# Kernel optimization log

Hardware: AMD Instinct MI355X
Metric: run time of the kernel (lower is better)

Reference implementation:

```python
import jax, jax.numpy as jnp
import numpy as np

B, D, T = 16384, 1024, 128  # batch, embed_dim, num_degradation_types
V, L = 4, 3                 # variants per sample, degradations per variant


def setup_inputs() -> dict:
    key = jax.random.key(0)
    k1, k2, k3, k4 = jax.random.split(key, 4)
    clean_embeddings = jax.random.normal(k1, (B, D), dtype=jnp.float32)
    W = jax.random.normal(k2, (T, D), dtype=jnp.float32) * (1.0 / np.sqrt(D))
    b = jnp.zeros((T,), dtype=jnp.float32)
    deg_indices = jax.random.randint(k3, (B, V, L), 0, T, dtype=jnp.int32)
    deg_mask = jax.random.randint(k4, (B, V, L), 0, 2, dtype=jnp.int32)
    return {"clean_embeddings": clean_embeddings, "W": W, "b": b,
            "deg_indices": deg_indices, "deg_mask": deg_mask}


def reference(clean_embeddings, W, b, deg_indices, deg_mask):
    # Linear + softmax: [B, T]
    logits = jnp.einsum("bd,td->bt", clean_embeddings, W) + b
    probs = jax.nn.softmax(logits, axis=-1)
    # Gather probs at each (batch, label) pair: [B, V*L] -> [B, V, L]
    flat_idx = deg_indices.reshape(B, V * L)
    gathered = jnp.take_along_axis(probs, flat_idx, axis=1).reshape(B, V, L)
    # Masked sum over all labels of a sample, divided by max(num_variants, 1)=V
    per_sample = (gathered * deg_mask.astype(probs.dtype)).sum(axis=(1, 2)) / V
    return per_sample.sum() / B
```

## Files before the change

kernel.cpp:

```cpp
#include <hip/hip_runtime.h>

#define B_SIZE 16384
#define D_DIM  1024
#define T_DIM  128
#define VLn    12
#define ROWS   16
#define KPW    256
#define NCHUNK 8

typedef __attribute__((ext_vector_type(8))) short  short8;
typedef __attribute__((ext_vector_type(4))) float  f32x4;

__device__ __forceinline__ unsigned short f2bf(float f) {
    union { float f; unsigned int u; } c; c.f = f;
    unsigned int u = c.u;
    return (unsigned short)((u + 0x7FFFu + ((u >> 16) & 1u)) >> 16);
}

__global__ __launch_bounds__(256)
void conv_w_kernel(const float* __restrict__ W, unsigned short* __restrict__ Wb) {
    const int i = (blockIdx.x * 256 + threadIdx.x) * 4;
    const float4 v = *(const float4*)(W + i);
    ushort4 h; h.x = f2bf(v.x); h.y = f2bf(v.y); h.z = f2bf(v.z); h.w = f2bf(v.w);
    *(ushort4*)(Wb + i) = h;
}

__global__ __launch_bounds__(256, 4)
void qloss_kernel(const float* __restrict__ emb,
                  const unsigned short* __restrict__ Wb,
                  const float* __restrict__ bias,
                  const int*   __restrict__ didx,
                  const int*   __restrict__ dmsk,
                  float*       __restrict__ out)
{
    __shared__ float sP[4 * 16 * 132 + 4];
    const int t    = threadIdx.x;
    const int w    = t >> 6;
    const int lane = t & 63;
    const int m15  = lane & 15;
    const int quad = lane >> 4;
    const int r0   = blockIdx.x * ROWS;

    f32x4 acc[8];
#pragma unroll
    for (int ct = 0; ct < 8; ++ct) acc[ct] = (f32x4){0.f, 0.f, 0.f, 0.f};

    const float*          aptr = emb + (size_t)(r0 + m15) * D_DIM + w * KPW + quad * 8;
    const unsigned short* bptr = Wb  + (size_t)m15 * D_DIM        + w * KPW + quad * 8;

#pragma unroll 2
    for (int kc = 0; kc < NCHUNK; ++kc) {
        const int ko = kc * 32;
        const float4 a0 = *(const float4*)(aptr + ko);
        const float4 a1 = *(const float4*)(aptr + ko + 4);
        short8 bf[8];
#pragma unroll
        for (int ct = 0; ct < 8; ++ct)
            bf[ct] = *(const short8*)(bptr + (size_t)ct * 16 * D_DIM + ko);
        short8 a;
        a[0] = (short)f2bf(a0.x); a[1] = (short)f2bf(a0.y);
        a[2] = (short)f2bf(a0.z); a[3] = (short)f2bf(a0.w);
        a[4] = (short)f2bf(a1.x); a[5] = (short)f2bf(a1.y);
        a[6] = (short)f2bf(a1.z); a[7] = (short)f2bf(a1.w);
#pragma unroll
        for (int ct = 0; ct < 8; ++ct)
            acc[ct] = __builtin_amdgcn_mfma_f32_16x16x32_bf16(a, bf[ct], acc[ct], 0, 0, 0);
    }

#pragma unroll
    for (int ct = 0; ct < 8; ++ct)
#pragma unroll
        for (int i = 0; i < 4; ++i)
            sP[w * 2112 + (quad * 4 + i) * 132 + ct * 16 + m15] = acc[ct][i];
    __syncthreads();

    const int row = t >> 4;
    const int s   = t & 15;
    {
        float v[8];
#pragma unroll
        for (int j = 0; j < 8; ++j) v[j] = bias[s * 8 + j];
#pragma unroll
        for (int w2 = 0; w2 < 4; ++w2) {
            const float4 p0 = *(const float4*)&sP[w2 * 2112 + row * 132 + s * 8];
            const float4 p1 = *(const float4*)&sP[w2 * 2112 + row * 132 + s * 8 + 4];
            v[0] += p0.x; v[1] += p0.y; v[2] += p0.z; v[3] += p0.w;
            v[4] += p1.x; v[5] += p1.y; v[6] += p1.z; v[7] += p1.w;
        }
        float m = -1e30f;
#pragma unroll
        for (int j = 0; j < 8; ++j) m = fmaxf(m, v[j]);
#pragma unroll
        for (int off = 1; off < 16; off <<= 1) m = fmaxf(m, __shfl_xor(m, off));
        float ssum = 0.f;
#pragma unroll
        for (int j = 0; j < 8; ++j) { v[j] = __expf(v[j] - m); ssum += v[j]; }
#pragma unroll
        for (int off = 1; off < 16; off <<= 1) ssum += __shfl_xor(ssum, off);
        const float inv = 1.0f / ssum;
        float4 q0 = {v[0] * inv, v[1] * inv, v[2] * inv, v[3] * inv};
        float4 q1 = {v[4] * inv, v[5] * inv, v[6] * inv, v[7] * inv};
        *(float4*)&sP[row * 132 + s * 8]     = q0;
        *(float4*)&sP[row * 132 + s * 8 + 4] = q1;
    }
    __syncthreads();

    float p = 0.f;
    if (s < 12) {
        const int gi  = (r0 + row) * VLn + s;
        const int idx = didx[gi];
        const int mk  = dmsk[gi];
        p = mk ? sP[row * 132 + idx] : 0.f;
    }
#pragma unroll
    for (int off = 1; off < 64; off <<= 1) p += __shfl_xor(p, off);
    if (lane == 0) sP[4 * 2112 + w] = p;
    __syncthreads();
    if (t == 0) {
        const float tot = sP[8448] + sP[8449] + sP[8450] + sP[8451];
        atomicAdd(out, tot * (1.0f / 65536.0f));
    }
}

extern "C" void kernel_launch(void* const* d_in, const int* in_sizes, int n_in,
                              void* d_out, int out_size, void* d_ws, size_t ws_size,
                              hipStream_t stream) {
    const float* emb  = (const float*)d_in[0];
    const float* W    = (const float*)d_in[1];
    const float* bias = (const float*)d_in[2];
    const int*   didx = (const int*)d_in[3];
    const int*   dmsk = (const int*)d_in[4];
    float* out = (float*)d_out;
    unsigned short* Wb = (unsigned short*)d_ws;

    hipMemsetAsync(out, 0, sizeof(float), stream);
    conv_w_kernel<<<(T_DIM * D_DIM) / (256 * 4), 256, 0, stream>>>(W, Wb);
    qloss_kernel<<<B_SIZE / ROWS, 256, 0, stream>>>(emb, Wb, bias, didx, dmsk, out);
}
```

Before: 131.6 us.

## Process 32 rows per block with register-prefetched loads and LDS atomic reduction

Doubles the rows per block so each wave reuses its loaded bf16 W fragments across two 16-row MFMA tiles, which halves W traffic per output row. It adds software prefetching of the next K chunk's A and B operands into registers, and replaces the per-wave partial buffers plus a separate sum pass with LDS atomicAdd into a single bias-initialized logits tile. The larger register footprint lowers the occupancy target to 2 blocks per CU, and the LDS float atomics may serialize.

```diff
diff --git a/kernel.cpp b/kernel.cpp
--- a/kernel.cpp
+++ b/kernel.cpp
@@ -4,9 +4,10 @@
 #define D_DIM  1024
 #define T_DIM  128
 #define VLn    12
-#define ROWS   16
+#define ROWS   32
 #define KPW    256
 #define NCHUNK 8
+#define STRIDE 132
 
 typedef __attribute__((ext_vector_type(8))) short  short8;
 typedef __attribute__((ext_vector_type(4))) float  f32x4;
@@ -17,6 +18,15 @@
     return (unsigned short)((u + 0x7FFFu + ((u >> 16) & 1u)) >> 16);
 }
 
+__device__ __forceinline__ short8 pack_bf16(float4 a, float4 b) {
+    short8 r;
+    r[0] = (short)f2bf(a.x); r[1] = (short)f2bf(a.y);
+    r[2] = (short)f2bf(a.z); r[3] = (short)f2bf(a.w);
+    r[4] = (short)f2bf(b.x); r[5] = (short)f2bf(b.y);
+    r[6] = (short)f2bf(b.z); r[7] = (short)f2bf(b.w);
+    return r;
+}
+
 __global__ __launch_bounds__(256)
 void conv_w_kernel(const float* __restrict__ W, unsigned short* __restrict__ Wb) {
     const int i = (blockIdx.x * 256 + threadIdx.x) * 4;
@@ -25,7 +35,7 @@
     *(ushort4*)(Wb + i) = h;
 }
 
-__global__ __launch_bounds__(256, 4)
+__global__ __launch_bounds__(256, 2)
 void qloss_kernel(const float* __restrict__ emb,
                   const unsigned short* __restrict__ Wb,
                   const float* __restrict__ bias,
@@ -33,7 +43,7 @@
                   const int*   __restrict__ dmsk,
                   float*       __restrict__ out)
 {
-    __shared__ float sP[4 * 16 * 132 + 4];
+    __shared__ float sL[ROWS * STRIDE + 8];
     const int t    = threadIdx.x;
     const int w    = t >> 6;
     const int lane = t & 63;
@@ -41,83 +51,108 @@
     const int quad = lane >> 4;
     const int r0   = blockIdx.x * ROWS;
 
-    f32x4 acc[8];
 #pragma unroll
-    for (int ct = 0; ct < 8; ++ct) acc[ct] = (f32x4){0.f, 0.f, 0.f, 0.f};
+    for (int i = t; i < ROWS * T_DIM; i += 256) {
+        const int row = i >> 7, col = i & 127;
+        sL[row * STRIDE + col] = bias[col];
+    }
+    if (t < 8) sL[ROWS * STRIDE + t] = 0.f;
+    __syncthreads();
 
-    const float*          aptr = emb + (size_t)(r0 + m15) * D_DIM + w * KPW + quad * 8;
-    const unsigned short* bptr = Wb  + (size_t)m15 * D_DIM        + w * KPW + quad * 8;
+    f32x4 acc[2][8];
+#pragma unroll
+    for (int mt = 0; mt < 2; ++mt)
+#pragma unroll
+        for (int ct = 0; ct < 8; ++ct) acc[mt][ct] = (f32x4){0.f, 0.f, 0.f, 0.f};
 
-#pragma unroll 2
+    const float*          aptr0 = emb + (size_t)(r0 + m15) * D_DIM + w * KPW + quad * 8;
+    const float*          aptr1 = aptr0 + 16 * D_DIM;
+    const unsigned short* bptr  = Wb  + (size_t)m15 * D_DIM + w * KPW + quad * 8;
+
+    float4 x0 = *(const float4*)(aptr0);
+    float4 x1 = *(const float4*)(aptr0 + 4);
+    float4 y0 = *(const float4*)(aptr1);
+    float4 y1 = *(const float4*)(aptr1 + 4);
+    short8 bf[8];
+#pragma unroll
+    for (int ct = 0; ct < 8; ++ct)
+        bf[ct] = *(const short8*)(bptr + (size_t)ct * 16 * D_DIM);
+
+#pragma unroll
     for (int kc = 0; kc < NCHUNK; ++kc) {
-        const int ko = kc * 32;
-        const float4 a0 = *(const float4*)(aptr + ko);
-        const float4 a1 = *(const float4*)(aptr + ko + 4);
-        short8 bf[8];
+        const float4 cx0 = x0, cx1 = x1, cy0 = y0, cy1 = y1;
+        short8 cbf[8];
 #pragma unroll
-        for (int ct = 0; ct < 8; ++ct)
-            bf[ct] = *(const short8*)(bptr + (size_t)ct * 16 * D_DIM + ko);
-        short8 a;
-        a[0] = (short)f2bf(a0.x); a[1] = (short)f2bf(a0.y);
-        a[2] = (short)f2bf(a0.z); a[3] = (short)f2bf(a0.w);
-        a[4] = (short)f2bf(a1.x); a[5] = (short)f2bf(a1.y);
-        a[6] = (short)f2bf(a1.z); a[7] = (short)f2bf(a1.w);
+        for (int ct = 0; ct < 8; ++ct) cbf[ct] = bf[ct];
+        if (kc + 1 < NCHUNK) {
+            const int ko = (kc + 1) * 32;
+            x0 = *(const float4*)(aptr0 + ko);
+            x1 = *(const float4*)(aptr0 + ko + 4);
+            y0 = *(const float4*)(aptr1 + ko);
+            y1 = *(const float4*)(aptr1 + ko + 4);
 #pragma unroll
-        for (int ct = 0; ct < 8; ++ct)
-            acc[ct] = __builtin_amdgcn_mfma_f32_16x16x32_bf16(a, bf[ct], acc[ct], 0, 0, 0);
+            for (int ct = 0; ct < 8; ++ct)
+                bf[ct] = *(const short8*)(bptr + (size_t)ct * 16 * D_DIM + ko);
+        }
+        const short8 a0 = pack_bf16(cx0, cx1);
+        const short8 a1 = pack_bf16(cy0, cy1);
+#pragma unroll
+        for (int ct = 0; ct < 8; ++ct) {
+            acc[0][ct] = __builtin_amdgcn_mfma_f32_16x16x32_bf16(a0, cbf[ct], acc[0][ct], 0, 0, 0);
+            acc[1][ct] = __builtin_amdgcn_mfma_f32_16x16x32_bf16(a1, cbf[ct], acc[1][ct], 0, 0, 0);
+        }
     }
 
 #pragma unroll
-    for (int ct = 0; ct < 8; ++ct)
+    for (int mt = 0; mt < 2; ++mt)
 #pragma unroll
-        for (int i = 0; i < 4; ++i)
-            sP[w * 2112 + (quad * 4 + i) * 132 + ct * 16 + m15] = acc[ct][i];
+        for (int ct = 0; ct < 8; ++ct)
+#pragma unroll
+            for (int i = 0; i < 4; ++i)
+                atomicAdd(&sL[(mt * 16 + quad * 4 + i) * STRIDE + ct * 16 + m15],
+                          acc[mt][ct][i]);
     __syncthreads();
 
-    const int row = t >> 4;
-    const int s   = t & 15;
     {
-        float v[8];
+        const int row = t >> 3, s = t & 7;
+        float* base = &sL[row * STRIDE + s * 16];
+        float v[16];
 #pragma unroll
-        for (int j = 0; j < 8; ++j) v[j] = bias[s * 8 + j];
-#pragma unroll
-        for (int w2 = 0; w2 < 4; ++w2) {
-            const float4 p0 = *(const float4*)&sP[w2 * 2112 + row * 132 + s * 8];
-            const float4 p1 = *(const float4*)&sP[w2 * 2112 + row * 132 + s * 8 + 4];
-            v[0] += p0.x; v[1] += p0.y; v[2] += p0.z; v[3] += p0.w;
-            v[4] += p1.x; v[5] += p1.y; v[6] += p1.z; v[7] += p1.w;
-        }
+        for (int j = 0; j < 4; ++j) *(float4*)&v[j * 4] = *(const float4*)(base + j * 4);
         float m = -1e30f;
 #pragma unroll
-        for (int j = 0; j < 8; ++j) m = fmaxf(m, v[j]);
+        for (int j = 0; j < 16; ++j) m = fmaxf(m, v[j]);
 #pragma unroll
-        for (int off = 1; off < 16; off <<= 1) m = fmaxf(m, __shfl_xor(m, off));
+        for (int off = 1; off < 8; off <<= 1) m = fmaxf(m, __shfl_xor(m, off));
         float ssum = 0.f;
 #pragma unroll
-        for (int j = 0; j < 8; ++j) { v[j] = __expf(v[j] - m); ssum += v[j]; }
+        for (int j = 0; j < 16; ++j) { v[j] = __expf(v[j] - m); ssum += v[j]; }
 #pragma unroll
-        for (int off = 1; off < 16; off <<= 1) ssum += __shfl_xor(ssum, off);
+        for (int off = 1; off < 8; off <<= 1) ssum += __shfl_xor(ssum, off);
         const float inv = 1.0f / ssum;
-        float4 q0 = {v[0] * inv, v[1] * inv, v[2] * inv, v[3] * inv};
-        float4 q1 = {v[4] * inv, v[5] * inv, v[6] * inv, v[7] * inv};
-        *(float4*)&sP[row * 132 + s * 8]     = q0;
-        *(float4*)&sP[row * 132 + s * 8 + 4] = q1;
+#pragma unroll
+        for (int j = 0; j < 16; ++j) v[j] *= inv;
+#pragma unroll
+        for (int j = 0; j < 4; ++j) *(float4*)(base + j * 4) = *(const float4*)&v[j * 4];
     }
     __syncthreads();
 
     float p = 0.f;
-    if (s < 12) {
-        const int gi  = (r0 + row) * VLn + s;
+#pragma unroll
+    for (int i = t; i < ROWS * VLn; i += 256) {
+        const int gi  = r0 * VLn + i;
+        const int row = i / VLn;
         const int idx = didx[gi];
         const int mk  = dmsk[gi];
-        p = mk ? sP[row * 132 + idx] : 0.f;
+        p += mk ? sL[row * STRIDE + idx] : 0.f;
     }
 #pragma unroll
     for (int off = 1; off < 64; off <<= 1) p += __shfl_xor(p, off);
-    if (lane == 0) sP[4 * 2112 + w] = p;
+    if (lane == 0) sL[ROWS * STRIDE + w] = p;
     __syncthreads();
     if (t == 0) {
-        const float tot = sP[8448] + sP[8449] + sP[8450] + sP[8451];
+        const float tot = sL[ROWS * STRIDE] + sL[ROWS * STRIDE + 1]
+                        + sL[ROWS * STRIDE + 2] + sL[ROWS * STRIDE + 3];
         atomicAdd(out, tot * (1.0f / 65536.0f));
     }
 }
```

Result: slower. 163.2 us (+24.1%).
